# Kernel tuning notes

Measured on AMD Instinct MI355X. Metric: run time of the kernel, lower is better.

Reference implementation:

```python
import jax, jax.numpy as jnp
import numpy as np

FP8_MAX = 448.0  # max finite value of float8_e4m3fn


def setup_inputs() -> dict:
    key = jax.random.key(0)
    k1, k2, k3 = jax.random.split(key, 3)
    T, H = 8192, 4096
    x = jax.random.normal(k1, (T, H), dtype=jnp.float32)
    w = jax.random.uniform(k2, (H, H), dtype=jnp.float32)  # stored as fp8 in the module; quantized in reference
    wscale = jax.random.uniform(k3, (1,), dtype=jnp.float32)
    return {"x": x, "w": w, "wscale": wscale}


def reference(x, w, wscale):
    # Dynamic per-token activation quantization to fp8 e4m3 (symmetric).
    x_scale = jnp.max(jnp.abs(x), axis=-1, keepdims=True) / FP8_MAX  # [T, 1]
    x_scale = jnp.maximum(x_scale, jnp.float32(1e-12))
    x_q = jnp.clip(x / x_scale, -FP8_MAX, FP8_MAX).astype(jnp.float8_e4m3fn)
    # Weight is stored in fp8 (per-tensor scale wscale); replicate the cast.
    w_q = w.astype(jnp.float8_e4m3fn)
    # Scaled fp8 matmul with fp32 accumulation, then dequant by x_scale * wscale.
    y = jnp.einsum('tk,kh->th', x_q.astype(jnp.float32), w_q.astype(jnp.float32))
    y = y * x_scale * wscale  # [T, H]
    # tensor_model_parallel_all_reduce is identity on a single device.
    return y
```

## Files before the change

kernel.cpp:

```cpp
#include <hip/hip_runtime.h>
#include <stdint.h>

#define T_DIM 8192
#define K_DIM 4096
#define N_DIM 4096
#define FP8MAX 448.0f
#define NT     32
#define BUFB   32768u

typedef __attribute__((ext_vector_type(4))) float floatx4;
typedef __attribute__((ext_vector_type(4))) int   intx4;
typedef __attribute__((ext_vector_type(8))) int   intx8;


__device__ static inline void load16_g2lds(const void* gptr, void* lptr) {
    __builtin_amdgcn_global_load_lds(
        (const __attribute__((address_space(1))) void*)gptr,
        (__attribute__((address_space(3))) void*)lptr,
        16, 0, 0);
}

__device__ static inline uint32_t pack4_fp8(float f0, float f1, float f2, float f3) {
    int p = 0;
    p = __builtin_amdgcn_cvt_pk_fp8_f32(f0, f1, p, false);
    p = __builtin_amdgcn_cvt_pk_fp8_f32(f2, f3, p, true);
    return (uint32_t)p;
}

__global__ __launch_bounds__(256) void quant_fused_kernel(
    const float* __restrict__ x, const float* __restrict__ w,
    uint8_t* __restrict__ xq, uint8_t* __restrict__ wqT,
    float* __restrict__ xscale)
{
    const int tid = threadIdx.x;
    if (blockIdx.x < T_DIM) {
        const int t = blockIdx.x;
        const int lane = tid & 63;
        const int wave = tid >> 6;
        const float4* xr4 = (const float4*)(x + (size_t)t * K_DIM);

        float4 v[4];
        float m = 0.0f;
#pragma unroll
        for (int e = 0; e < 4; ++e) {
            v[e] = xr4[tid + e * 256];
            m = fmaxf(m, fmaxf(fmaxf(fabsf(v[e].x), fabsf(v[e].y)),
                               fmaxf(fabsf(v[e].z), fabsf(v[e].w))));
        }
#pragma unroll
        for (int off = 32; off > 0; off >>= 1)
            m = fmaxf(m, __shfl_down(m, off, 64));
        __shared__ float red[4];
        if (lane == 0) red[wave] = m;
        __syncthreads();
        float mm = fmaxf(fmaxf(red[0], red[1]), fmaxf(red[2], red[3]));
        float scale = fmaxf(mm / FP8MAX, 1e-12f);
        if (tid == 0) xscale[t] = scale;
        const float inv = 1.0f / scale;

        uint32_t* xqr = (uint32_t*)(xq + (size_t)t * K_DIM);
#pragma unroll
        for (int e = 0; e < 4; ++e) {
            float q0 = fminf(fmaxf(v[e].x * inv, -FP8MAX), FP8MAX);
            float q1 = fminf(fmaxf(v[e].y * inv, -FP8MAX), FP8MAX);
            float q2 = fminf(fmaxf(v[e].z * inv, -FP8MAX), FP8MAX);
            float q3 = fminf(fmaxf(v[e].w * inv, -FP8MAX), FP8MAX);
            xqr[tid + e * 256] = pack4_fp8(q0, q1, q2, q3);
        }
    } else {
        const int b = blockIdx.x - T_DIM;
        const int n0 = (b & 63) * 64;
        const int k0 = (b >> 6) * 64;
        __shared__ uint32_t tile[64][17];

#pragma unroll
        for (int e = 0; e < 4; ++e) {
            int idx = tid + e * 256;
            int r = idx >> 4;
            int c4 = idx & 15;
            float4 v = *(const float4*)(w + (size_t)(k0 + r) * N_DIM + n0 + c4 * 4);
            tile[r][c4] = pack4_fp8(v.x, v.y, v.z, v.w);
        }
        __syncthreads();
        const int kg = tid & 15;
        const int ng = tid >> 4;
        uint32_t in0 = tile[kg * 4 + 0][ng];
        uint32_t in1 = tile[kg * 4 + 1][ng];
        uint32_t in2 = tile[kg * 4 + 2][ng];
        uint32_t in3 = tile[kg * 4 + 3][ng];
#pragma unroll
        for (int i = 0; i < 4; ++i) {
            uint32_t o = ((in0 >> (8 * i)) & 0xFFu)
                       | (((in1 >> (8 * i)) & 0xFFu) << 8)
                       | (((in2 >> (8 * i)) & 0xFFu) << 16)
                       | (((in3 >> (8 * i)) & 0xFFu) << 24);
            *(uint32_t*)(wqT + (size_t)(n0 + ng * 4 + i) * K_DIM + k0 + kg * 4) = o;
        }
    }
}

__global__ __launch_bounds__(256, 3) void gemm_fp8_kernel(
    const uint8_t* __restrict__ xq, const uint8_t* __restrict__ wqT,
    const float* __restrict__ xscale, const float* __restrict__ wscale,
    float* __restrict__ out)
{
    __shared__ __align__(16) uint8_t lds[2 * BUFB];

    const int tid  = threadIdx.x;
    const int lane = tid & 63;
    const int wave = tid >> 6;
    const int m0 = blockIdx.y * 128;
    const int n0 = blockIdx.x * 128;
    const int wm = (wave >> 1) * 64;
    const int wn = (wave & 1) * 64;
    const int row  = lane & 15;
    const int quad = lane >> 4;

    floatx4 acc[4][4] = {{{0.f,0.f,0.f,0.f}}};

    const uint8_t* gA[4];
    const uint8_t* gB[4];
    uint32_t lA[4], lB[4];
#pragma unroll
    for (int p = 0; p < 4; ++p) {
        const int c = tid + p * 256;
        const int r = c >> 3, gg = c & 7, g = gg ^ (r & 7);
        gA[p] = xq  + (size_t)(m0 + r) * K_DIM + g * 16;
        gB[p] = wqT + (size_t)(n0 + r) * K_DIM + g * 16;
        lA[p] = (uint32_t)c * 16u;
        lB[p] = 16384u + (uint32_t)c * 16u;
    }

    int aoff0[4], aoff1[4], boff0[4], boff1[4];
#pragma unroll
    for (int i = 0; i < 4; ++i) {
        const int mr = wm + i * 16 + row;
        const int nr = wn + i * 16 + row;
        aoff0[i] = mr * 128 + (((2 * quad)     ^ (mr & 7)) << 4);
        aoff1[i] = mr * 128 + (((2 * quad + 1) ^ (mr & 7)) << 4);
        boff0[i] = 16384 + nr * 128 + (((2 * quad)     ^ (nr & 7)) << 4);
        boff1[i] = 16384 + nr * 128 + (((2 * quad + 1) ^ (nr & 7)) << 4);
    }

#define READ_A(i) { \
    intx4 lo = *(const intx4*)(Ab + aoff0[i]); \
    intx4 hi = *(const intx4*)(Ab + aoff1[i]); \
    a[i] = __builtin_shufflevector(lo, hi, 0, 1, 2, 3, 4, 5, 6, 7); }
#define READ_B(j) { \
    intx4 lo = *(const intx4*)(Ab + boff0[j]); \
    intx4 hi = *(const intx4*)(Ab + boff1[j]); \
    b[j] = __builtin_shufflevector(lo, hi, 0, 1, 2, 3, 4, 5, 6, 7); }
#define MFMA_ROW(i) \
    acc[i][0] = __builtin_amdgcn_mfma_scale_f32_16x16x128_f8f6f4(a[i], b[0], acc[i][0], 0, 0, 0, 0x7F7F7F7F, 0, 0x7F7F7F7F); \
    acc[i][1] = __builtin_amdgcn_mfma_scale_f32_16x16x128_f8f6f4(a[i], b[1], acc[i][1], 0, 0, 0, 0x7F7F7F7F, 0, 0x7F7F7F7F); \
    acc[i][2] = __builtin_amdgcn_mfma_scale_f32_16x16x128_f8f6f4(a[i], b[2], acc[i][2], 0, 0, 0, 0x7F7F7F7F, 0, 0x7F7F7F7F); \
    acc[i][3] = __builtin_amdgcn_mfma_scale_f32_16x16x128_f8f6f4(a[i], b[3], acc[i][3], 0, 0, 0, 0x7F7F7F7F, 0, 0x7F7F7F7F);

#pragma unroll
    for (int p = 0; p < 4; ++p) {
        load16_g2lds(gA[p], &lds[lA[p]]);
        load16_g2lds(gB[p], &lds[lB[p]]);
    }
    __syncthreads();

    for (int t = 0; t < NT; ++t) {
        if (t < NT - 1) {
            const uint32_t nb = (uint32_t)((t + 1) & 1) * BUFB;
            const int kk = (t + 1) * 128;
#pragma unroll
            for (int p = 0; p < 4; ++p) {
                load16_g2lds(gA[p] + kk, &lds[nb + lA[p]]);
                load16_g2lds(gB[p] + kk, &lds[nb + lB[p]]);
            }
        }

        const uint8_t* Ab = &lds[(uint32_t)(t & 1) * BUFB];
        intx8 a[4], b[4];
        READ_A(0); READ_A(1); READ_A(2); READ_A(3);
        READ_B(0); READ_B(1); READ_B(2); READ_B(3);
        __builtin_amdgcn_s_setprio(1);
        MFMA_ROW(0); MFMA_ROW(1); MFMA_ROW(2); MFMA_ROW(3);
        __builtin_amdgcn_s_setprio(0);

        __syncthreads();
    }

    const float wsv = wscale[0];
#pragma unroll
    for (int i = 0; i < 4; ++i) {
        const int rbase = m0 + wm + i * 16 + quad * 4;
        float s[4];
#pragma unroll
        for (int r = 0; r < 4; ++r) s[r] = xscale[rbase + r] * wsv;
#pragma unroll
        for (int j = 0; j < 4; ++j) {
            const int col = n0 + wn + j * 16 + row;
#pragma unroll
            for (int r = 0; r < 4; ++r)
                out[(size_t)(rbase + r) * N_DIM + col] = acc[i][j][r] * s[r];
        }
    }
#undef READ_A
#undef READ_B
#undef MFMA_ROW
}


extern "C" void kernel_launch(void* const* d_in, const int* in_sizes, int n_in,
                              void* d_out, int out_size, void* d_ws, size_t ws_size,
                              hipStream_t stream) {
    const float* x      = (const float*)d_in[0];
    const float* w      = (const float*)d_in[1];
    const float* wscale = (const float*)d_in[2];
    float* out = (float*)d_out;

    uint8_t* xq  = (uint8_t*)d_ws;
    uint8_t* wqT = xq + (size_t)T_DIM * K_DIM;
    float* xscale = (float*)(wqT + (size_t)N_DIM * K_DIM);

    quant_fused_kernel<<<T_DIM + (N_DIM / 64) * (K_DIM / 64), 256, 0, stream>>>(
        x, w, xq, wqT, xscale);
    gemm_fp8_kernel<<<dim3(N_DIM / 128, T_DIM / 128), 256, 0, stream>>>(
        xq, wqT, xscale, wscale, out);
}
```

Before: 395.6 us.

## Enlarge FP8 GEMM block tile to 256x256 with 512 threads

```diff
diff --git a/kernel.cpp b/kernel.cpp
--- a/kernel.cpp
+++ b/kernel.cpp
@@ -6,7 +6,7 @@
 #define N_DIM 4096
 #define FP8MAX 448.0f
 #define NT     32
-#define BUFB   32768u
+#define BUFB   65536u
 
 typedef __attribute__((ext_vector_type(4))) float floatx4;
 typedef __attribute__((ext_vector_type(4))) int   intx4;
@@ -99,7 +99,7 @@
     }
 }
 
-__global__ __launch_bounds__(256, 3) void gemm_fp8_kernel(
+__global__ __launch_bounds__(512, 2) void gemm_fp8_kernel(
     const uint8_t* __restrict__ xq, const uint8_t* __restrict__ wqT,
     const float* __restrict__ xscale, const float* __restrict__ wscale,
     float* __restrict__ out)
@@ -109,77 +109,63 @@
     const int tid  = threadIdx.x;
     const int lane = tid & 63;
     const int wave = tid >> 6;
-    const int m0 = blockIdx.y * 128;
-    const int n0 = blockIdx.x * 128;
-    const int wm = (wave >> 1) * 64;
-    const int wn = (wave & 1) * 64;
+    const int m0 = blockIdx.y * 256;
+    const int n0 = blockIdx.x * 256;
+    const int wm = (wave >> 2) * 128;
+    const int wn = (wave & 3) * 64;
     const int row  = lane & 15;
     const int quad = lane >> 4;
 
-    floatx4 acc[4][4] = {{{0.f,0.f,0.f,0.f}}};
-
-    const uint8_t* gA[4];
-    const uint8_t* gB[4];
-    uint32_t lA[4], lB[4];
-#pragma unroll
-    for (int p = 0; p < 4; ++p) {
-        const int c = tid + p * 256;
-        const int r = c >> 3, gg = c & 7, g = gg ^ (r & 7);
-        gA[p] = xq  + (size_t)(m0 + r) * K_DIM + g * 16;
-        gB[p] = wqT + (size_t)(n0 + r) * K_DIM + g * 16;
-        lA[p] = (uint32_t)c * 16u;
-        lB[p] = 16384u + (uint32_t)c * 16u;
-    }
-
-    int aoff0[4], aoff1[4], boff0[4], boff1[4];
-#pragma unroll
-    for (int i = 0; i < 4; ++i) {
-        const int mr = wm + i * 16 + row;
-        const int nr = wn + i * 16 + row;
-        aoff0[i] = mr * 128 + (((2 * quad)     ^ (mr & 7)) << 4);
-        aoff1[i] = mr * 128 + (((2 * quad + 1) ^ (mr & 7)) << 4);
-        boff0[i] = 16384 + nr * 128 + (((2 * quad)     ^ (nr & 7)) << 4);
-        boff1[i] = 16384 + nr * 128 + (((2 * quad + 1) ^ (nr & 7)) << 4);
-    }
-
-#define READ_A(i) { \
-    intx4 lo = *(const intx4*)(Ab + aoff0[i]); \
-    intx4 hi = *(const intx4*)(Ab + aoff1[i]); \
-    a[i] = __builtin_shufflevector(lo, hi, 0, 1, 2, 3, 4, 5, 6, 7); }
+    floatx4 acc[8][4] = {{{0.f,0.f,0.f,0.f}}};
+
+    const int r0 = tid >> 3;
+    const int g0 = (tid & 7) ^ (r0 & 7);
+    const uint8_t* gAb = xq  + (size_t)(m0 + r0) * K_DIM + g0 * 16;
+    const uint8_t* gBb = wqT + (size_t)(n0 + r0) * K_DIM + g0 * 16;
+    const uint32_t lA0 = (uint32_t)tid * 16u;
+    const uint32_t lB0 = 32768u + (uint32_t)tid * 16u;
+
+    const int slot = ((2 * quad) ^ (row & 7)) << 4;
+    const int abase = (wm + row) * 128 + slot;
+    const int bbase = 32768 + (wn + row) * 128 + slot;
+
+#define STAGE(kk, nb) do { \
+    _Pragma("unroll") \
+    for (int p = 0; p < 4; ++p) { \
+        load16_g2lds(gAb + (size_t)p * 64 * K_DIM + (kk), &lds[(nb) + lA0 + p * 8192u]); \
+        load16_g2lds(gBb + (size_t)p * 64 * K_DIM + (kk), &lds[(nb) + lB0 + p * 8192u]); \
+    } } while (0)
+
+#define READ_A(d, i) { \
+    intx4 lo = *(const intx4*)(Ab + abase + (i) * 2048); \
+    intx4 hi = *(const intx4*)(Ab + (abase ^ 16) + (i) * 2048); \
+    a[d] = __builtin_shufflevector(lo, hi, 0, 1, 2, 3, 4, 5, 6, 7); }
 #define READ_B(j) { \
-    intx4 lo = *(const intx4*)(Ab + boff0[j]); \
-    intx4 hi = *(const intx4*)(Ab + boff1[j]); \
+    intx4 lo = *(const intx4*)(Ab + bbase + (j) * 2048); \
+    intx4 hi = *(const intx4*)(Ab + (bbase ^ 16) + (j) * 2048); \
     b[j] = __builtin_shufflevector(lo, hi, 0, 1, 2, 3, 4, 5, 6, 7); }
-#define MFMA_ROW(i) \
-    acc[i][0] = __builtin_amdgcn_mfma_scale_f32_16x16x128_f8f6f4(a[i], b[0], acc[i][0], 0, 0, 0, 0x7F7F7F7F, 0, 0x7F7F7F7F); \
-    acc[i][1] = __builtin_amdgcn_mfma_scale_f32_16x16x128_f8f6f4(a[i], b[1], acc[i][1], 0, 0, 0, 0x7F7F7F7F, 0, 0x7F7F7F7F); \
-    acc[i][2] = __builtin_amdgcn_mfma_scale_f32_16x16x128_f8f6f4(a[i], b[2], acc[i][2], 0, 0, 0, 0x7F7F7F7F, 0, 0x7F7F7F7F); \
-    acc[i][3] = __builtin_amdgcn_mfma_scale_f32_16x16x128_f8f6f4(a[i], b[3], acc[i][3], 0, 0, 0, 0x7F7F7F7F, 0, 0x7F7F7F7F);
-
-#pragma unroll
-    for (int p = 0; p < 4; ++p) {
-        load16_g2lds(gA[p], &lds[lA[p]]);
-        load16_g2lds(gB[p], &lds[lB[p]]);
-    }
+#define MFMA4(i, d) \
+    acc[i][0] = __builtin_amdgcn_mfma_scale_f32_16x16x128_f8f6f4(a[d], b[0], acc[i][0], 0, 0, 0, 0x7F7F7F7F, 0, 0x7F7F7F7F); \
+    acc[i][1] = __builtin_amdgcn_mfma_scale_f32_16x16x128_f8f6f4(a[d], b[1], acc[i][1], 0, 0, 0, 0x7F7F7F7F, 0, 0x7F7F7F7F); \
+    acc[i][2] = __builtin_amdgcn_mfma_scale_f32_16x16x128_f8f6f4(a[d], b[2], acc[i][2], 0, 0, 0, 0x7F7F7F7F, 0, 0x7F7F7F7F); \
+    acc[i][3] = __builtin_amdgcn_mfma_scale_f32_16x16x128_f8f6f4(a[d], b[3], acc[i][3], 0, 0, 0, 0x7F7F7F7F, 0, 0x7F7F7F7F);
+
+    STAGE(0, 0u);
     __syncthreads();
 
     for (int t = 0; t < NT; ++t) {
-        if (t < NT - 1) {
-            const uint32_t nb = (uint32_t)((t + 1) & 1) * BUFB;
-            const int kk = (t + 1) * 128;
-#pragma unroll
-            for (int p = 0; p < 4; ++p) {
-                load16_g2lds(gA[p] + kk, &lds[nb + lA[p]]);
-                load16_g2lds(gB[p] + kk, &lds[nb + lB[p]]);
-            }
-        }
+        if (t < NT - 1) STAGE((t + 1) * 128, (uint32_t)((t + 1) & 1) * BUFB);
 
         const uint8_t* Ab = &lds[(uint32_t)(t & 1) * BUFB];
         intx8 a[4], b[4];
-        READ_A(0); READ_A(1); READ_A(2); READ_A(3);
         READ_B(0); READ_B(1); READ_B(2); READ_B(3);
+        READ_A(0, 0); READ_A(1, 1); READ_A(2, 2); READ_A(3, 3);
         __builtin_amdgcn_s_setprio(1);
-        MFMA_ROW(0); MFMA_ROW(1); MFMA_ROW(2); MFMA_ROW(3);
+        MFMA4(0, 0); MFMA4(1, 1); MFMA4(2, 2); MFMA4(3, 3);
+        __builtin_amdgcn_s_setprio(0);
+        READ_A(0, 4); READ_A(1, 5); READ_A(2, 6); READ_A(3, 7);
+        __builtin_amdgcn_s_setprio(1);
+        MFMA4(4, 0); MFMA4(5, 1); MFMA4(6, 2); MFMA4(7, 3);
         __builtin_amdgcn_s_setprio(0);
 
         __syncthreads();
@@ -187,7 +173,7 @@
 
     const float wsv = wscale[0];
 #pragma unroll
-    for (int i = 0; i < 4; ++i) {
+    for (int i = 0; i < 8; ++i) {
         const int rbase = m0 + wm + i * 16 + quad * 4;
         float s[4];
 #pragma unroll
@@ -200,9 +186,10 @@
                 out[(size_t)(rbase + r) * N_DIM + col] = acc[i][j][r] * s[r];
         }
     }
+#undef STAGE
 #undef READ_A
 #undef READ_B
-#undef MFMA_ROW
+#undef MFMA4
 }
 
 
@@ -220,6 +207,6 @@
 
     quant_fused_kernel<<<T_DIM + (N_DIM / 64) * (K_DIM / 64), 256, 0, stream>>>(
         x, w, xq, wqT, xscale);
-    gemm_fp8_kernel<<<dim3(N_DIM / 128, T_DIM / 128), 256, 0, stream>>>(
+    gemm_fp8_kernel<<<dim3(N_DIM / 256, T_DIM / 256), 512, 0, stream>>>(
         xq, wqT, xscale, wscale, out);
 }
```

Result: faster. 385.4 us (-2.6%).
